# Kernel optimization log

Measured on AMD Instinct MI355X. Metric: run time of the kernel, lower is better.

Reference implementation:

```python
import jax, jax.numpy as jnp
import numpy as np

N_ANCH = 100800   # 3 * (160^2 + 80^2 + 40^2), YOLOv5 @ 1280
NUM_CLS = 80
IMG_HW = 1280
MAX_DETS = 300    # fixed padding for jit-compatible NMS output
OUT = 224
SCORE_THRESH = 0.1
IOU_THRESH = 0.45
ALLOWED = jnp.array([1, 2, 3, 4, 6, 8, 17, 18, 44], dtype=jnp.int32)
MEAN = jnp.array([0.485, 0.456, 0.406], dtype=jnp.float32).reshape(1, 3, 1, 1)
STD = jnp.array([0.229, 0.224, 0.225], dtype=jnp.float32).reshape(1, 3, 1, 1)


def setup_inputs() -> dict:
    key = jax.random.key(0)
    k1, k2, k3, k4, k5 = jax.random.split(key, 5)
    # realistic YOLO-style raw predictions: cx,cy in-image, modest w,h, gaussian class logits
    cxcy = jax.random.uniform(k1, (1, 2, N_ANCH), dtype=jnp.float32) * IMG_HW
    wh = jax.random.uniform(k2, (1, 2, N_ANCH), dtype=jnp.float32) * 256.0 + 8.0
    obj = jax.random.uniform(k3, (1, 1, N_ANCH), dtype=jnp.float32)
    logits = jax.random.normal(k4, (1, NUM_CLS, N_ANCH), dtype=jnp.float32)
    raw_pred = jnp.concatenate([cxcy, wh, obj, logits], axis=1)  # [1, 5+C, N]
    image = jax.random.uniform(k5, (1, 3, IMG_HW, IMG_HW), dtype=jnp.float32)
    return {"raw_pred": raw_pred, "image": image}


def _pairwise_iou(b):
    # b: [K,4] xyxy
    area = (b[:, 2] - b[:, 0]) * (b[:, 3] - b[:, 1])
    lt = jnp.maximum(b[:, None, :2], b[None, :, :2])
    rb = jnp.minimum(b[:, None, 2:], b[None, :, 2:])
    wh = jnp.clip(rb - lt, 0.0)
    inter = wh[..., 0] * wh[..., 1]
    union = area[:, None] + area[None, :] - inter
    return inter / jnp.maximum(union, 1e-9)


def _nms_keep(iou, valid):
    # greedy NMS over score-sorted boxes; returns boolean keep mask [K]
    K = iou.shape[0]
    idx = jnp.arange(K)

    def body(i, keep):
        suppress = keep[i] & (iou[i] > IOU_THRESH) & (idx > i)
        return keep & ~suppress

    return jax.lax.fori_loop(0, K, body, valid)


def _roi_align(image_chw, boxes):
    # torchvision roi_align, aligned=True, one sample per bin at the bin center
    # (sampling_ratio fixed to 1; see notes). image_chw: [3,H,W], boxes: [M,4]
    C, H, W = image_chw.shape
    grid = (jnp.arange(OUT, dtype=jnp.float32) + 0.5) / OUT  # fractional bin centers

    def one(box):
        x1, y1, x2, y2 = box
        xs = x1 - 0.5 + grid * (x2 - x1)  # [OUT], aligned=True half-pixel offset
        ys = y1 - 0.5 + grid * (y2 - y1)
        vx = (xs >= -1.0) & (xs <= W)
        vy = (ys >= -1.0) & (ys <= H)
        xc = jnp.clip(xs, 0.0, W - 1)
        yc = jnp.clip(ys, 0.0, H - 1)
        x0 = jnp.floor(xc).astype(jnp.int32)
        y0 = jnp.floor(yc).astype(jnp.int32)
        x1i = jnp.minimum(x0 + 1, W - 1)
        y1i = jnp.minimum(y0 + 1, H - 1)
        lx = xc - x0
        ly = yc - y0
        # bilinear gather: [3, OUT, OUT]
        v00 = image_chw[:, y0[:, None], x0[None, :]]
        v01 = image_chw[:, y0[:, None], x1i[None, :]]
        v10 = image_chw[:, y1i[:, None], x0[None, :]]
        v11 = image_chw[:, y1i[:, None], x1i[None, :]]
        top = v00 * (1.0 - lx) + v01 * lx
        bot = v10 * (1.0 - lx) + v11 * lx
        val = top * (1.0 - ly)[None, :, None] + bot * ly[None, :, None]
        return jnp.where(vy[None, :, None] & vx[None, None, :], val, 0.0)

    return jax.vmap(one)(boxes)


def _forward(raw_pred, image):
    x = raw_pred[0].T  # [N, 5+C]
    cx, cy, w, h = x[:, 0], x[:, 1], x[:, 2], x[:, 3]
    boxes = jnp.stack([cx - w / 2, cy - h / 2, cx + w / 2, cy + h / 2], axis=1)
    cls_logits = x[:, 5:]
    scores = cls_logits.max(axis=1)
    classes = cls_logits.argmax(axis=1).astype(jnp.int32) + 1
    # score + allowed-class filter (mask form)
    mask = (scores > SCORE_THRESH) & jnp.isin(classes, ALLOWED)
    masked_scores = jnp.where(mask, scores, jnp.finfo(scores.dtype).min)
    top_scores, top_idx = jax.lax.top_k(masked_scores, MAX_DETS)  # sorted desc
    top_boxes = boxes[top_idx]
    top_classes = classes[top_idx]
    valid = mask[top_idx]
    # greedy NMS over padded top-K candidates
    keep = _nms_keep(_pairwise_iou(top_boxes), valid)
    final_boxes = jnp.where(keep[:, None], top_boxes, 0.0)
    final_scores = jnp.where(keep, top_scores, 0.0)
    final_classes = jnp.where(keep, top_classes, 0)
    # crops: full image first, then RoIAlign crops, normalized once
    full_crop = jax.image.resize(image, (1, 3, OUT, OUT), method='linear', antialias=False)
    roi_crops = _roi_align(image[0], final_boxes)  # [K,3,224,224]
    roi_crops = jnp.where(keep[:, None, None, None], roi_crops, 0.0)
    all_crops = jnp.concatenate([full_crop, roi_crops], axis=0)  # [K+1,3,224,224]
    all_crops = (all_crops - MEAN) / STD
    return final_boxes, final_scores, final_classes, all_crops, keep


def reference(raw_pred, image):
    return _forward(raw_pred, image)
```

## Files before the change

### kernel.cpp

```cpp
#include <hip/hip_runtime.h>
#include <stdint.h>

#define N_ANCH   100800
#define NUM_CLS  80
#define IMG_HW   1280
#define MAX_DETS 300
#define OUTSZ    224
#define CAND_CAP 4096
#define LIST_CAP 16384

#define OFF_BOXES   0
#define OFF_SCORES  1200
#define OFF_CLASSES 1500
#define OFF_CROPS   1800
#define CROPS_ELEMS (301 * 3 * 224 * 224)
#define OFF_KEEP    (OFF_CROPS + CROPS_ELEMS)

#define SC_CNT    0
#define SC_CAND   64

typedef float f32x4 __attribute__((ext_vector_type(4)));

__device__ __forceinline__ uint32_t fkey(float f) {
    uint32_t u = __float_as_uint(f);
    return (u & 0x80000000u) ? ~u : (u | 0x80000000u);
}
__device__ __forceinline__ float unfkey(uint32_t k) {
    uint32_t u = (k & 0x80000000u) ? (k & 0x7fffffffu) : ~k;
    return __uint_as_float(u);
}

__global__ void k_score(const float* __restrict__ rp,
                        unsigned long long* __restrict__ cand,
                        uint32_t* __restrict__ cnt) {
    int gid = blockIdx.x * 256 + threadIdx.x;
    int grp = gid >> 3;
    int cp  = gid & 7;
    bool in = (grp < N_ANCH / 4);
    int a4 = in ? grp * 4 : 0;

    float best[4] = {-3.402823466e38f, -3.402823466e38f, -3.402823466e38f, -3.402823466e38f};
    int   bc[4]   = {0, 0, 0, 0};
    #pragma unroll
    for (int k = 0; k < 10; ++k) {
        int c = cp + 8 * k;
        float4 v = *(const float4*)&rp[(size_t)(5 + c) * N_ANCH + a4];
        if (v.x > best[0]) { best[0] = v.x; bc[0] = c; }
        if (v.y > best[1]) { best[1] = v.y; bc[1] = c; }
        if (v.z > best[2]) { best[2] = v.z; bc[2] = c; }
        if (v.w > best[3]) { best[3] = v.w; bc[3] = c; }
    }
    #pragma unroll
    for (int m = 1; m < 8; m <<= 1) {
        #pragma unroll
        for (int j = 0; j < 4; ++j) {
            float ob = __shfl_xor(best[j], m);
            int   oc = __shfl_xor(bc[j], m);
            if (ob > best[j] || (ob == best[j] && oc < bc[j])) { best[j] = ob; bc[j] = oc; }
        }
    }

    const unsigned long long AM =
        (1ULL << 1) | (1ULL << 2) | (1ULL << 3) | (1ULL << 4) | (1ULL << 6) |
        (1ULL << 8) | (1ULL << 17) | (1ULL << 18) | (1ULL << 44);
    unsigned long long pk[4];
    int cnt_loc = 0;
    bool lead = (cp == 0) && in;
    #pragma unroll
    for (int k = 0; k < 4; ++k) {
        int cls = bc[k] + 1;
        bool mk = lead && (best[k] > 0.1f) && (cls < 64) && ((AM >> cls) & 1ULL);
        uint32_t low = ((0x1FFFFu ^ (uint32_t)(a4 + k)) << 7) | (uint32_t)cls;
        pk[k] = mk ? (((unsigned long long)fkey(best[k]) << 32) | low) : 0ull;
        cnt_loc += mk ? 1 : 0;
    }

    int inc = cnt_loc;
    #pragma unroll
    for (int d = 1; d < 64; d <<= 1) {
        int vv = __shfl_up(inc, d);
        if ((threadIdx.x & 63) >= d) inc += vv;
    }
    int total = __shfl(inc, 63);
    uint32_t base = 0u;
    if (((threadIdx.x & 63) == 63) && total > 0) base = atomicAdd(cnt, (uint32_t)total);
    base = (uint32_t)__shfl((int)base, 63);
    uint32_t pos = base + (uint32_t)(inc - cnt_loc);
    #pragma unroll
    for (int k = 0; k < 4; ++k) {
        if (pk[k]) {
            if (pos < LIST_CAP) cand[pos] = pk[k];
            ++pos;
        }
    }
}

__global__ void __launch_bounds__(1024) k_detect(const float* __restrict__ rp,
                                                 const unsigned long long* __restrict__ cand,
                                                 const uint32_t* __restrict__ cnt_p,
                                                 float* __restrict__ out) {
    __shared__ uint32_t lhist[16384];
    __shared__ uint32_t ssum[1024];
    __shared__ uint32_t swave[16];
    __shared__ int      sh_thr;
    __shared__ uint32_t s_cnt;
    __shared__ unsigned long long sb[CAND_CAP];
    __shared__ unsigned long long top[MAX_DETS];
    __shared__ float sbx[MAX_DETS][4];
    __shared__ float sscore[MAX_DETS];
    __shared__ int   scls[MAX_DETS];
    __shared__ __align__(8) uint32_t sup[MAX_DETS][10];
    __shared__ __align__(8) uint32_t kw[10];
    __shared__ __align__(8) uint32_t rnz[10];
    int t = threadIdx.x;
    int nl = min((int)(*cnt_p), LIST_CAP);

    #pragma unroll
    for (int i = 0; i < 16; ++i) lhist[t + i * 1024] = 0u;
    if (t == 0) s_cnt = 0u;
    __syncthreads();
    for (int i = t; i < nl; i += 1024)
        atomicAdd(&lhist[(uint32_t)(cand[i] >> 50)], 1u);
    __syncthreads();

    const uint4* h4 = (const uint4*)(&lhist[t * 16]);
    uint4 v0 = h4[0], v1 = h4[1], v2 = h4[2], v3 = h4[3];
    uint32_t s = v0.x + v0.y + v0.z + v0.w + v1.x + v1.y + v1.z + v1.w +
                 v2.x + v2.y + v2.z + v2.w + v3.x + v3.y + v3.z + v3.w;
    ssum[t] = s;
    uint32_t ws = s;
    #pragma unroll
    for (int m = 32; m; m >>= 1) ws += __shfl_xor(ws, m);
    if ((t & 63) == 0) swave[t >> 6] = ws;
    __syncthreads();
    if (t == 0) {
        uint32_t acc = 0; int wsel = -1;
        for (int w = 15; w >= 0; --w) {
            uint32_t v = swave[w];
            if (acc + v >= (uint32_t)MAX_DETS) { wsel = w; break; }
            acc += v;
        }
        int thr = 0;
        if (wsel >= 0) {
            int tsel = -1;
            for (int tg = wsel * 64 + 63; tg >= wsel * 64; --tg) {
                uint32_t v = ssum[tg];
                if (acc + v >= (uint32_t)MAX_DETS) { tsel = tg; break; }
                acc += v;
            }
            for (int b = tsel * 16 + 15; b >= tsel * 16; --b) {
                acc += lhist[b];
                if (acc >= (uint32_t)MAX_DETS) { thr = b; break; }
            }
        }
        sh_thr = thr;
    }
    __syncthreads();

    uint32_t thr = (uint32_t)sh_thr;
    for (int i = t; i < nl; i += 1024) {
        unsigned long long key = cand[i];
        if ((uint32_t)(key >> 50) >= thr) {
            uint32_t pos = atomicAdd(&s_cnt, 1u);
            if (pos < CAND_CAP) sb[pos] = key;
        }
    }
    __syncthreads();
    int n = min((int)s_cnt, CAND_CAP);

    if (t < MAX_DETS) top[t] = 0ull;
    for (int i = t; i < MAX_DETS * 10; i += 1024) ((uint32_t*)sup)[i] = 0u;
    if (t < 10) { kw[t] = 0u; rnz[t] = 0u; }
    __syncthreads();

    for (int i = t; i < n; i += 1024) {
        unsigned long long key = sb[i];
        int rank = 0;
        for (int j = 0; j < n; ++j) rank += (sb[j] > key) ? 1 : 0;
        if (rank < MAX_DETS) top[rank] = key;
    }
    __syncthreads();

    if (t < MAX_DETS) {
        unsigned long long key = top[t];
        bool valid = (key != 0ull);
        float score = 0.f; int cls = 0;
        float b0 = 0.f, b1 = 0.f, b2 = 0.f, b3 = 0.f;
        if (valid) {
            uint32_t low = (uint32_t)key;
            uint32_t a = 0x1FFFFu ^ ((low >> 7) & 0x1FFFFu);
            cls = (int)(low & 0x7Fu);
            score = unfkey((uint32_t)(key >> 32));
            float cx = rp[a], cy = rp[N_ANCH + a];
            float w = rp[2 * N_ANCH + a], h = rp[3 * N_ANCH + a];
            b0 = cx - w * 0.5f; b1 = cy - h * 0.5f;
            b2 = cx + w * 0.5f; b3 = cy + h * 0.5f;
            atomicOr(&kw[t >> 5], 1u << (t & 31));
        }
        sbx[t][0] = b0; sbx[t][1] = b1; sbx[t][2] = b2; sbx[t][3] = b3;
        sscore[t] = score; scls[t] = cls;
    }
    __syncthreads();

    for (int p = t; p < MAX_DETS * MAX_DETS; p += 1024) {
        int i = p / MAX_DETS, j = p % MAX_DETS;
        if (j > i) {
            float ax1 = sbx[i][0], ay1 = sbx[i][1], ax2 = sbx[i][2], ay2 = sbx[i][3];
            float bx1 = sbx[j][0], by1 = sbx[j][1], bx2 = sbx[j][2], by2 = sbx[j][3];
            float areaA = (ax2 - ax1) * (ay2 - ay1);
            float areaB = (bx2 - bx1) * (by2 - by1);
            float ltx = fmaxf(ax1, bx1), lty = fmaxf(ay1, by1);
            float rbx = fminf(ax2, bx2), rby = fminf(ay2, by2);
            float iw = fmaxf(rbx - ltx, 0.f), ih = fmaxf(rby - lty, 0.f);
            float inter = iw * ih;
            float uni = areaA + areaB - inter;
            float iou = inter / fmaxf(uni, 1e-9f);
            if (iou > 0.45f) {
                atomicOr(&sup[i][j >> 5], 1u << (j & 31));
                atomicOr(&rnz[i >> 5], 1u << (i & 31));
            }
        }
    }
    __syncthreads();

    if (t == 0) {
        unsigned long long kwr[5], rnzr[5];
        const unsigned long long* kq = (const unsigned long long*)kw;
        const unsigned long long* rq = (const unsigned long long*)rnz;
        #pragma unroll
        for (int w = 0; w < 5; ++w) { kwr[w] = kq[w]; rnzr[w] = rq[w]; }
        #pragma unroll
        for (int sblk = 0; sblk < 5; ++sblk) {
            int lim = (sblk == 4) ? (MAX_DETS - 4 * 64) : 64;
            for (int i2 = 0; i2 < lim; ++i2) {
                if (((kwr[sblk] >> i2) & 1ull) && ((rnzr[sblk] >> i2) & 1ull)) {
                    int i = sblk * 64 + i2;
                    const unsigned long long* row = (const unsigned long long*)&sup[i][0];
                    kwr[0] &= ~row[0]; kwr[1] &= ~row[1]; kwr[2] &= ~row[2];
                    kwr[3] &= ~row[3]; kwr[4] &= ~row[4];
                }
            }
        }
        unsigned long long* kqo = (unsigned long long*)kw;
        #pragma unroll
        for (int w = 0; w < 5; ++w) kqo[w] = kwr[w];
    }
    __syncthreads();

    if (t < MAX_DETS) {
        bool kp = (kw[t >> 5] >> (t & 31)) & 1u;
        out[OFF_BOXES + t * 4 + 0] = kp ? sbx[t][0] : 0.f;
        out[OFF_BOXES + t * 4 + 1] = kp ? sbx[t][1] : 0.f;
        out[OFF_BOXES + t * 4 + 2] = kp ? sbx[t][2] : 0.f;
        out[OFF_BOXES + t * 4 + 3] = kp ? sbx[t][3] : 0.f;
        out[OFF_SCORES + t]  = kp ? sscore[t] : 0.f;
        out[OFF_CLASSES + t] = kp ? (float)scls[t] : 0.f;
        out[OFF_KEEP + t]    = kp ? 1.f : 0.f;
    }
}

#define TROWS  8
#define TPITCH 272

__device__ __forceinline__ float bilerp_g(const float* __restrict__ ch, float xc, float yc) {
    int x0 = (int)floorf(xc), y0 = (int)floorf(yc);
    int x1 = min(x0 + 1, IMG_HW - 1), y1 = min(y0 + 1, IMG_HW - 1);
    float lx = xc - (float)x0, ly = yc - (float)y0;
    float v00 = ch[y0 * IMG_HW + x0], v01 = ch[y0 * IMG_HW + x1];
    float v10 = ch[y1 * IMG_HW + x0], v11 = ch[y1 * IMG_HW + x1];
    return (v00 * (1.f - lx) + v01 * lx) * (1.f - ly) +
           (v10 * (1.f - lx) + v11 * lx) * ly;
}

__global__ void k_crops(const float* __restrict__ img, float* __restrict__ out) {
    __shared__ float tile[TROWS * TPITCH];
    int bx = blockIdx.x;
    int nc = blockIdx.y;
    int n = nc / 3, c = nc - n * 3;
    int t = threadIdx.x;
    int q = bx * 256 + t;
    int oy = q / 56;
    int ox0 = (q - oy * 56) * 4;
    const float meanv[3] = {0.485f, 0.456f, 0.406f};
    const float stdv[3]  = {0.229f, 0.224f, 0.225f};
    float mean = meanv[c], rstd = 1.0f / stdv[c];
    const float* ch = img + (size_t)c * (IMG_HW * IMG_HW);
    f32x4 v;

    if (n == 0) {
        float sy = ((float)oy + 0.5f) * (1280.0f / 224.0f) - 0.5f;
        #pragma unroll
        for (int k = 0; k < 4; ++k) {
            float sx = ((float)(ox0 + k) + 0.5f) * (1280.0f / 224.0f) - 0.5f;
            v[k] = (bilerp_g(ch, sx, sy) - mean) * rstd;
        }
    } else {
        float kp = out[OFF_KEEP + (n - 1)];
        if (kp == 0.f) {
            float z = (0.f - mean) * rstd;
            v = (f32x4){z, z, z, z};
        } else {
            float4 bxv = *(const float4*)&out[OFF_BOXES + (n - 1) * 4];
            float x1b = bxv.x, y1b = bxv.y, x2b = bxv.z, y2b = bxv.w;
            float bw = x2b - x1b, bh = y2b - y1b;
            float x1bm = x1b - 0.5f, y1bm = y1b - 0.5f;
            int oy_s = (bx * 256) / 56;
            int oy_e = (bx * 256 + 255) / 56;
            float ys0 = y1bm + (((float)oy_s + 0.5f) / 224.0f) * bh;
            float ys1 = y1bm + (((float)oy_e + 0.5f) / 224.0f) * bh;
            float xs0 = x1bm + (0.5f / 224.0f) * bw;
            float xs1 = x1bm + (223.5f / 224.0f) * bw;
            int iy_min = (int)floorf(fminf(fmaxf(ys0, 0.f), 1279.f));
            int iy_max = min((int)floorf(fminf(fmaxf(ys1, 0.f), 1279.f)) + 1, IMG_HW - 1);
            int ix_min = (int)floorf(fminf(fmaxf(xs0, 0.f), 1279.f));
            int ix_max = min((int)floorf(fminf(fmaxf(xs1, 0.f), 1279.f)) + 1, IMG_HW - 1);
            int ix_al = ix_min & ~3;
            int rows = iy_max - iy_min + 1;
            int w4   = (ix_max - ix_al + 4) >> 2;
            int total = rows * w4;
            float winv = 1.0f / (float)w4;
            for (int i = t; i < total; i += 256) {
                int r  = (int)((float)i * winv);
                int cc = i - r * w4;
                if (cc < 0)        { r--; cc += w4; }
                else if (cc >= w4) { r++; cc -= w4; }
                int gy = iy_min + r;
                int px = ix_al + cc * 4;
                const float* src = ch + (size_t)gy * IMG_HW + px;
                float4 val;
                if ((px + 3 < IMG_HW) || (gy < IMG_HW - 1) || (c < 2)) {
                    val = *(const float4*)src;
                } else {
                    val.x = src[0];
                    val.y = src[min(1, IMG_HW - 1 - px)];
                    val.z = src[min(2, IMG_HW - 1 - px)];
                    val.w = src[min(3, IMG_HW - 1 - px)];
                }
                *(float4*)&tile[r * TPITCH + cc * 4] = val;
            }
            __syncthreads();

            bool interior = (xs0 >= 0.0f) && (xs1 < 1279.0f) &&
                            (ys0 >= 0.0f) && (ys1 < 1279.0f);
            float gy = ((float)oy + 0.5f) / 224.0f;
            float ys = y1bm + gy * bh;
            if (interior) {
                float y0f = floorf(ys);
                float ly = ys - y0f;
                int y0 = (int)y0f;
                int ry0 = (y0 - iy_min) * TPITCH - ix_al;
                int ry1 = ry0 + TPITCH;
                #pragma unroll
                for (int k = 0; k < 4; ++k) {
                    float gx = ((float)(ox0 + k) + 0.5f) / 224.0f;
                    float xs = x1bm + gx * bw;
                    float x0f = floorf(xs);
                    float lx = xs - x0f;
                    int x0 = (int)x0f;
                    int a0 = ry0 + x0, a1 = ry1 + x0;
                    float t00 = tile[a0], t01 = tile[a0 + 1];
                    float t10 = tile[a1], t11 = tile[a1 + 1];
                    float top = __builtin_fmaf(lx, t01 - t00, t00);
                    float bot = __builtin_fmaf(lx, t11 - t10, t10);
                    float val = __builtin_fmaf(ly, bot - top, top);
                    v[k] = (val - mean) * rstd;
                }
            } else {
                bool vy = (ys >= -1.0f) && (ys <= 1280.0f);
                float ycl = fminf(fmaxf(ys, 0.f), 1279.f);
                int y0 = (int)floorf(ycl);
                int y1i = min(y0 + 1, IMG_HW - 1);
                float ly = ycl - (float)y0;
                int ry0 = (y0 - iy_min) * TPITCH - ix_al;
                int ry1 = (y1i - iy_min) * TPITCH - ix_al;
                #pragma unroll
                for (int k = 0; k < 4; ++k) {
                    float gx = ((float)(ox0 + k) + 0.5f) / 224.0f;
                    float xs = x1bm + gx * bw;
                    bool vx = (xs >= -1.0f) && (xs <= 1280.0f);
                    float xcl = fminf(fmaxf(xs, 0.f), 1279.f);
                    int x0 = (int)floorf(xcl);
                    int x1i = min(x0 + 1, IMG_HW - 1);
                    float lx = xcl - (float)x0;
                    float v00 = tile[ry0 + x0], v01 = tile[ry0 + x1i];
                    float v10 = tile[ry1 + x0], v11 = tile[ry1 + x1i];
                    float val = (v00 * (1.f - lx) + v01 * lx) * (1.f - ly) +
                                (v10 * (1.f - lx) + v11 * lx) * ly;
                    if (!(vx && vy)) val = 0.f;
                    v[k] = (val - mean) * rstd;
                }
            }
        }
    }
    f32x4* dst = (f32x4*)(out + OFF_CROPS + (size_t)nc * (OUTSZ * OUTSZ) + oy * OUTSZ + ox0);
    __builtin_nontemporal_store(v, dst);
}

extern "C" void kernel_launch(void* const* d_in, const int* in_sizes, int n_in,
                              void* d_out, int out_size, void* d_ws, size_t ws_size,
                              hipStream_t stream) {
    (void)in_sizes; (void)n_in; (void)out_size; (void)d_ws; (void)ws_size;
    const float* rp  = (const float*)d_in[0];
    const float* img = (const float*)d_in[1];
    float* out = (float*)d_out;
    char* sbase = (char*)d_out + (size_t)OFF_CROPS * sizeof(float);
    uint32_t* cnt = (uint32_t*)(sbase + SC_CNT);
    unsigned long long* cand = (unsigned long long*)(sbase + SC_CAND);

    hipMemsetAsync(sbase, 0, 64, stream);
    k_score<<<(N_ANCH / 4 * 8 + 255) / 256, 256, 0, stream>>>(rp, cand, cnt);
    k_detect<<<1, 1024, 0, stream>>>(rp, cand, cnt, out);
    dim3 grid(49, 903);
    k_crops<<<grid, 256, 0, stream>>>(img, out);
}
```

Baseline: 344.0 us.

## Process all three channels per crop block to reuse box setup

The crop kernel now launches one block per crop and loops over the three color channels inside it, instead of one block per crop-channel pair. Box bounds, tile extents, interpolation weights and tile addresses are computed once and reused for every channel, and normalization becomes a single FMA. The aim is to cut redundant per-block setup and the keep/box loads while tripling the work per block. The tradeoff is a third as many blocks, plus an extra barrier and serialized tile loads per channel, which may reduce latency hiding. The separate interior fast path is dropped in favour of the general clamped path.

Measured after the change: 327.0 us. 1.05x faster.

```diff
diff --git a/kernel.cpp b/kernel.cpp
--- a/kernel.cpp
+++ b/kernel.cpp
@@ -262,138 +262,141 @@
 #define TROWS  8
 #define TPITCH 272
 
-__device__ __forceinline__ float bilerp_g(const float* __restrict__ ch, float xc, float yc) {
-    int x0 = (int)floorf(xc), y0 = (int)floorf(yc);
-    int x1 = min(x0 + 1, IMG_HW - 1), y1 = min(y0 + 1, IMG_HW - 1);
-    float lx = xc - (float)x0, ly = yc - (float)y0;
-    float v00 = ch[y0 * IMG_HW + x0], v01 = ch[y0 * IMG_HW + x1];
-    float v10 = ch[y1 * IMG_HW + x0], v11 = ch[y1 * IMG_HW + x1];
-    return (v00 * (1.f - lx) + v01 * lx) * (1.f - ly) +
-           (v10 * (1.f - lx) + v11 * lx) * ly;
-}
-
 __global__ void k_crops(const float* __restrict__ img, float* __restrict__ out) {
     __shared__ float tile[TROWS * TPITCH];
     int bx = blockIdx.x;
-    int nc = blockIdx.y;
-    int n = nc / 3, c = nc - n * 3;
+    int n  = blockIdx.y;
     int t = threadIdx.x;
     int q = bx * 256 + t;
     int oy = q / 56;
     int ox0 = (q - oy * 56) * 4;
-    const float meanv[3] = {0.485f, 0.456f, 0.406f};
-    const float stdv[3]  = {0.229f, 0.224f, 0.225f};
-    float mean = meanv[c], rstd = 1.0f / stdv[c];
-    const float* ch = img + (size_t)c * (IMG_HW * IMG_HW);
-    f32x4 v;
+    const float scl[3] = {1.0f / 0.229f, 1.0f / 0.224f, 1.0f / 0.225f};
+    const float bia[3] = {-0.485f / 0.229f, -0.456f / 0.224f, -0.406f / 0.225f};
+    size_t obase = (size_t)OFF_CROPS + (size_t)(n * 3) * (OUTSZ * OUTSZ)
+                 + (size_t)oy * OUTSZ + ox0;
 
     if (n == 0) {
         float sy = ((float)oy + 0.5f) * (1280.0f / 224.0f) - 0.5f;
+        int y0 = (int)floorf(sy);
+        float ly = sy - (float)y0;
+        int x0a[4]; float lxa[4];
         #pragma unroll
         for (int k = 0; k < 4; ++k) {
             float sx = ((float)(ox0 + k) + 0.5f) * (1280.0f / 224.0f) - 0.5f;
-            v[k] = (bilerp_g(ch, sx, sy) - mean) * rstd;
-        }
-    } else {
-        float kp = out[OFF_KEEP + (n - 1)];
-        if (kp == 0.f) {
-            float z = (0.f - mean) * rstd;
-            v = (f32x4){z, z, z, z};
-        } else {
-            float4 bxv = *(const float4*)&out[OFF_BOXES + (n - 1) * 4];
-            float x1b = bxv.x, y1b = bxv.y, x2b = bxv.z, y2b = bxv.w;
-            float bw = x2b - x1b, bh = y2b - y1b;
-            float x1bm = x1b - 0.5f, y1bm = y1b - 0.5f;
-            int oy_s = (bx * 256) / 56;
-            int oy_e = (bx * 256 + 255) / 56;
-            float ys0 = y1bm + (((float)oy_s + 0.5f) / 224.0f) * bh;
-            float ys1 = y1bm + (((float)oy_e + 0.5f) / 224.0f) * bh;
-            float xs0 = x1bm + (0.5f / 224.0f) * bw;
-            float xs1 = x1bm + (223.5f / 224.0f) * bw;
-            int iy_min = (int)floorf(fminf(fmaxf(ys0, 0.f), 1279.f));
-            int iy_max = min((int)floorf(fminf(fmaxf(ys1, 0.f), 1279.f)) + 1, IMG_HW - 1);
-            int ix_min = (int)floorf(fminf(fmaxf(xs0, 0.f), 1279.f));
-            int ix_max = min((int)floorf(fminf(fmaxf(xs1, 0.f), 1279.f)) + 1, IMG_HW - 1);
-            int ix_al = ix_min & ~3;
-            int rows = iy_max - iy_min + 1;
-            int w4   = (ix_max - ix_al + 4) >> 2;
-            int total = rows * w4;
-            float winv = 1.0f / (float)w4;
-            for (int i = t; i < total; i += 256) {
-                int r  = (int)((float)i * winv);
-                int cc = i - r * w4;
-                if (cc < 0)        { r--; cc += w4; }
-                else if (cc >= w4) { r++; cc -= w4; }
-                int gy = iy_min + r;
-                int px = ix_al + cc * 4;
-                const float* src = ch + (size_t)gy * IMG_HW + px;
-                float4 val;
-                if ((px + 3 < IMG_HW) || (gy < IMG_HW - 1) || (c < 2)) {
-                    val = *(const float4*)src;
-                } else {
-                    val.x = src[0];
-                    val.y = src[min(1, IMG_HW - 1 - px)];
-                    val.z = src[min(2, IMG_HW - 1 - px)];
-                    val.w = src[min(3, IMG_HW - 1 - px)];
-                }
-                *(float4*)&tile[r * TPITCH + cc * 4] = val;
-            }
-            __syncthreads();
-
-            bool interior = (xs0 >= 0.0f) && (xs1 < 1279.0f) &&
-                            (ys0 >= 0.0f) && (ys1 < 1279.0f);
-            float gy = ((float)oy + 0.5f) / 224.0f;
-            float ys = y1bm + gy * bh;
-            if (interior) {
-                float y0f = floorf(ys);
-                float ly = ys - y0f;
-                int y0 = (int)y0f;
-                int ry0 = (y0 - iy_min) * TPITCH - ix_al;
-                int ry1 = ry0 + TPITCH;
-                #pragma unroll
-                for (int k = 0; k < 4; ++k) {
-                    float gx = ((float)(ox0 + k) + 0.5f) / 224.0f;
-                    float xs = x1bm + gx * bw;
-                    float x0f = floorf(xs);
-                    float lx = xs - x0f;
-                    int x0 = (int)x0f;
-                    int a0 = ry0 + x0, a1 = ry1 + x0;
-                    float t00 = tile[a0], t01 = tile[a0 + 1];
-                    float t10 = tile[a1], t11 = tile[a1 + 1];
-                    float top = __builtin_fmaf(lx, t01 - t00, t00);
-                    float bot = __builtin_fmaf(lx, t11 - t10, t10);
-                    float val = __builtin_fmaf(ly, bot - top, top);
-                    v[k] = (val - mean) * rstd;
-                }
+            x0a[k] = (int)floorf(sx);
+            lxa[k] = sx - floorf(sx);
+        }
+        #pragma unroll
+        for (int c = 0; c < 3; ++c) {
+            const float* r0 = img + (size_t)c * (IMG_HW * IMG_HW) + (size_t)y0 * IMG_HW;
+            const float* r1 = r0 + IMG_HW;
+            f32x4 v;
+            #pragma unroll
+            for (int k = 0; k < 4; ++k) {
+                float t00 = r0[x0a[k]], t01 = r0[x0a[k] + 1];
+                float t10 = r1[x0a[k]], t11 = r1[x0a[k] + 1];
+                float top = __builtin_fmaf(lxa[k], t01 - t00, t00);
+                float bot = __builtin_fmaf(lxa[k], t11 - t10, t10);
+                float val = __builtin_fmaf(ly, bot - top, top);
+                v[k] = __builtin_fmaf(val, scl[c], bia[c]);
+            }
+            __builtin_nontemporal_store(v, (f32x4*)(out + obase + (size_t)c * (OUTSZ * OUTSZ)));
+        }
+        return;
+    }
+
+    float kp = out[OFF_KEEP + (n - 1)];
+    if (kp == 0.f) {
+        #pragma unroll
+        for (int c = 0; c < 3; ++c) {
+            f32x4 v = (f32x4){bia[c], bia[c], bia[c], bia[c]};
+            __builtin_nontemporal_store(v, (f32x4*)(out + obase + (size_t)c * (OUTSZ * OUTSZ)));
+        }
+        return;
+    }
+
+    float4 bxv = *(const float4*)&out[OFF_BOXES + (n - 1) * 4];
+    float x1b = bxv.x, y1b = bxv.y, x2b = bxv.z, y2b = bxv.w;
+    float bw = x2b - x1b, bh = y2b - y1b;
+    float x1bm = x1b - 0.5f, y1bm = y1b - 0.5f;
+    int oy_s = (bx * 256) / 56;
+    int oy_e = (bx * 256 + 255) / 56;
+    float ys0 = y1bm + (((float)oy_s + 0.5f) / 224.0f) * bh;
+    float ys1 = y1bm + (((float)oy_e + 0.5f) / 224.0f) * bh;
+    float xs0 = x1bm + (0.5f / 224.0f) * bw;
+    float xs1 = x1bm + (223.5f / 224.0f) * bw;
+    int iy_min = (int)floorf(fminf(fmaxf(ys0, 0.f), 1279.f));
+    int iy_max = min((int)floorf(fminf(fmaxf(ys1, 0.f), 1279.f)) + 1, IMG_HW - 1);
+    int ix_min = (int)floorf(fminf(fmaxf(xs0, 0.f), 1279.f));
+    int ix_max = min((int)floorf(fminf(fmaxf(xs1, 0.f), 1279.f)) + 1, IMG_HW - 1);
+    int ix_al = ix_min & ~3;
+    int rows = iy_max - iy_min + 1;
+    int w4   = (ix_max - ix_al + 4) >> 2;
+    int total = rows * w4;
+    float winv = 1.0f / (float)w4;
+
+    float gy = ((float)oy + 0.5f) / 224.0f;
+    float ys = y1bm + gy * bh;
+    bool vy = (ys >= -1.0f) && (ys <= 1280.0f);
+    float ycl = fminf(fmaxf(ys, 0.f), 1279.f);
+    int y0 = (int)floorf(ycl);
+    int y1i = min(y0 + 1, IMG_HW - 1);
+    float ly = ycl - (float)y0;
+    int rb0 = (y0 - iy_min) * TPITCH - ix_al;
+    int rb1 = (y1i - iy_min) * TPITCH - ix_al;
+    int a0a[4], a1a[4];
+    int d1a[4];
+    float lxa[4]; bool oka[4];
+    #pragma unroll
+    for (int k = 0; k < 4; ++k) {
+        float gx = ((float)(ox0 + k) + 0.5f) / 224.0f;
+        float xs = x1bm + gx * bw;
+        oka[k] = vy && (xs >= -1.0f) && (xs <= 1280.0f);
+        float xcl = fminf(fmaxf(xs, 0.f), 1279.f);
+        int x0 = (int)floorf(xcl);
+        int x1i = min(x0 + 1, IMG_HW - 1);
+        lxa[k] = xcl - (float)x0;
+        a0a[k] = rb0 + x0;
+        a1a[k] = rb1 + x0;
+        d1a[k] = x1i - x0;
+    }
+
+    for (int c = 0; c < 3; ++c) {
+        if (c) __syncthreads();
+        const float* ch = img + (size_t)c * (IMG_HW * IMG_HW);
+        for (int i = t; i < total; i += 256) {
+            int r  = (int)((float)i * winv);
+            int cc = i - r * w4;
+            if (cc < 0)        { r--; cc += w4; }
+            else if (cc >= w4) { r++; cc -= w4; }
+            int gyr = iy_min + r;
+            int px = ix_al + cc * 4;
+            const float* src = ch + (size_t)gyr * IMG_HW + px;
+            float4 val;
+            if ((px + 3 < IMG_HW) || (gyr < IMG_HW - 1) || (c < 2)) {
+                val = *(const float4*)src;
             } else {
-                bool vy = (ys >= -1.0f) && (ys <= 1280.0f);
-                float ycl = fminf(fmaxf(ys, 0.f), 1279.f);
-                int y0 = (int)floorf(ycl);
-                int y1i = min(y0 + 1, IMG_HW - 1);
-                float ly = ycl - (float)y0;
-                int ry0 = (y0 - iy_min) * TPITCH - ix_al;
-                int ry1 = (y1i - iy_min) * TPITCH - ix_al;
-                #pragma unroll
-                for (int k = 0; k < 4; ++k) {
-                    float gx = ((float)(ox0 + k) + 0.5f) / 224.0f;
-                    float xs = x1bm + gx * bw;
-                    bool vx = (xs >= -1.0f) && (xs <= 1280.0f);
-                    float xcl = fminf(fmaxf(xs, 0.f), 1279.f);
-                    int x0 = (int)floorf(xcl);
-                    int x1i = min(x0 + 1, IMG_HW - 1);
-                    float lx = xcl - (float)x0;
-                    float v00 = tile[ry0 + x0], v01 = tile[ry0 + x1i];
-                    float v10 = tile[ry1 + x0], v11 = tile[ry1 + x1i];
-                    float val = (v00 * (1.f - lx) + v01 * lx) * (1.f - ly) +
-                                (v10 * (1.f - lx) + v11 * lx) * ly;
-                    if (!(vx && vy)) val = 0.f;
-                    v[k] = (val - mean) * rstd;
-                }
-            }
-        }
-    }
-    f32x4* dst = (f32x4*)(out + OFF_CROPS + (size_t)nc * (OUTSZ * OUTSZ) + oy * OUTSZ + ox0);
-    __builtin_nontemporal_store(v, dst);
+                val.x = src[0];
+                val.y = src[min(1, IMG_HW - 1 - px)];
+                val.z = src[min(2, IMG_HW - 1 - px)];
+                val.w = src[min(3, IMG_HW - 1 - px)];
+            }
+            *(float4*)&tile[r * TPITCH + cc * 4] = val;
+        }
+        __syncthreads();
+        f32x4 v;
+        #pragma unroll
+        for (int k = 0; k < 4; ++k) {
+            float t00 = tile[a0a[k]], t01 = tile[a0a[k] + d1a[k]];
+            float t10 = tile[a1a[k]], t11 = tile[a1a[k] + d1a[k]];
+            float top = __builtin_fmaf(lxa[k], t01 - t00, t00);
+            float bot = __builtin_fmaf(lxa[k], t11 - t10, t10);
+            float val = __builtin_fmaf(ly, bot - top, top);
+            if (!oka[k]) val = 0.f;
+            v[k] = __builtin_fmaf(val, scl[c], bia[c]);
+        }
+        __builtin_nontemporal_store(v, (f32x4*)(out + obase + (size_t)c * (OUTSZ * OUTSZ)));
+    }
 }
 
 extern "C" void kernel_launch(void* const* d_in, const int* in_sizes, int n_in,
@@ -410,6 +413,6 @@
     hipMemsetAsync(sbase, 0, 64, stream);
     k_score<<<(N_ANCH / 4 * 8 + 255) / 256, 256, 0, stream>>>(rp, cand, cnt);
     k_detect<<<1, 1024, 0, stream>>>(rp, cand, cnt, out);
-    dim3 grid(49, 903);
+    dim3 grid(49, 301);
     k_crops<<<grid, 256, 0, stream>>>(img, out);
 }
```
